# Performance work log

Measured on AMD Instinct MI355X. Metric: run time of the kernel, lower is better.

The kernel has to match this reference:

```python
import jax, jax.numpy as jnp
import numpy as np

NUM_EMBED = 1024
EMBED_DIM = 256
DECAY = 0.99
EPS = 1e-05
COMMIT = 0.25


def setup_inputs() -> dict:
    key = jax.random.key(0)
    k1, k2, k3 = jax.random.split(key, 3)
    z = jax.random.normal(k1, (64, 32, 32, EMBED_DIM), dtype=jnp.float32)
    lim = 1.0 / NUM_EMBED
    embeddings = jax.random.uniform(k2, (NUM_EMBED, EMBED_DIM), minval=-lim, maxval=lim, dtype=jnp.float32)
    ema_embed = jax.random.uniform(k3, (NUM_EMBED, EMBED_DIM), minval=-lim, maxval=lim, dtype=jnp.float32)
    cluster_size = jnp.zeros((NUM_EMBED,), dtype=jnp.float32)
    return {"z": z, "embeddings": embeddings, "ema_embed": ema_embed, "cluster_size": cluster_size}


def reference(z, embeddings, ema_embed, cluster_size):
    B, H, W, D = z.shape
    zf = z.reshape(-1, D)  # [N, D]
    # squared euclidean distances to codebook: [N, K]
    distances = (zf ** 2).sum(-1, keepdims=True) + (embeddings ** 2).sum(-1) - 2.0 * (zf @ embeddings.T)
    closest = jnp.argmin(distances, axis=-1)  # [N] int
    quantized_indices = closest.reshape(B, H, W)[:, None]  # [B,1,H,W]
    quantized = embeddings[closest].reshape(z.shape)  # gather instead of one-hot GEMM

    # --- training-mode EMA codebook update (buffer math, no grads) ---
    n_i = jnp.zeros((NUM_EMBED,), dtype=zf.dtype).at[closest].add(1.0)  # per-code counts
    new_cluster = cluster_size * DECAY + n_i * (1.0 - DECAY)
    dw = jnp.zeros_like(embeddings).at[closest].add(zf)  # scatter-add of assigned vectors
    new_ema = ema_embed * DECAY + dw * (1.0 - DECAY)
    n = new_cluster.sum()
    new_cluster = (new_cluster + EPS) / (n + NUM_EMBED * EPS) * n
    new_embeddings = new_ema / new_cluster[:, None]

    commitment_loss = jnp.mean((quantized - z) ** 2)
    st_quantized = z + jax.lax.stop_gradient(quantized - z)  # straight-through
    loss = commitment_loss * COMMIT
    return loss, st_quantized, quantized_indices, new_embeddings, new_cluster, new_ema
```

## Files before the change

kernel.cpp:

```cpp
#include <hip/hip_runtime.h>
#include <float.h>
#include <stdint.h>

#define K_EMB 1024
#define D_EMB 256

typedef _Float16 half8 __attribute__((ext_vector_type(8)));
typedef float f32x4_t __attribute__((ext_vector_type(4)));


__global__ void convert_e_kernel(const float* __restrict__ e, _Float16* __restrict__ ehp,
                                 float* __restrict__ t2, unsigned int* __restrict__ flag_cnt) {
  if (blockIdx.x == 0 && threadIdx.x == 0) { flag_cnt[0] = 0; flag_cnt[1] = 0; }
  int row = blockIdx.x * 4 + (threadIdx.x >> 6);
  int lane = threadIdx.x & 63;
  float4 v = ((const float4*)(e + (size_t)row * D_EMB))[lane];
  float s = v.x * v.x + v.y * v.y + v.z * v.z + v.w * v.w;
#pragma unroll
  for (int off = 32; off > 0; off >>= 1) s += __shfl_down(s, off, 64);
  if (lane == 0) t2[row] = s;
  _Float16* dst = ehp + (size_t)row * D_EMB + lane * 4;
  dst[0] = (_Float16)v.x; dst[1] = (_Float16)v.y;
  dst[2] = (_Float16)v.z; dst[3] = (_Float16)v.w;
}


#define BM 256
#define CCH 64
#define NCH (K_EMB / CCH)
#define DELTA 1.5e-4f

__launch_bounds__(512, 2)
__global__ void argmin_mfma_kernel(const float* __restrict__ z,
                                   const _Float16* __restrict__ eh,
                                   const float* __restrict__ t2,
                                   int* __restrict__ closest,
                                   float* __restrict__ idx_out,
                                   unsigned int* __restrict__ flag_cnt,
                                   unsigned int* __restrict__ flag_row,
                                   unsigned int* __restrict__ flag_cand) {
  __shared__ _Float16 ebuf[2 * CCH * D_EMB];
  const int tid = threadIdx.x;
  const int wid = tid >> 6;
  const int lane = tid & 63;
  const int c = lane & 15, g = lane >> 4;
  const int row0 = blockIdx.x * BM + wid * 32;

  half8 A[2][8];
#pragma unroll
  for (int fr = 0; fr < 2; ++fr)
#pragma unroll
    for (int df = 0; df < 8; ++df) {
      const float* zp = z + (size_t)(row0 + fr * 16 + c) * D_EMB + df * 32 + g * 8;
      const float4 v0 = *(const float4*)zp;
      const float4 v1 = *(const float4*)(zp + 4);
      half8 h;
      h[0] = (_Float16)v0.x; h[1] = (_Float16)v0.y; h[2] = (_Float16)v0.z; h[3] = (_Float16)v0.w;
      h[4] = (_Float16)v1.x; h[5] = (_Float16)v1.y; h[6] = (_Float16)v1.z; h[7] = (_Float16)v1.w;
      A[fr][df] = h;
    }

  float m1[8], m2[8], m3[8];
  int k1[8], k2[8];
#pragma unroll
  for (int s = 0; s < 8; ++s) { m1[s] = FLT_MAX; m2[s] = FLT_MAX; m3[s] = FLT_MAX; k1[s] = 0; k2[s] = 0; }

#define INS(s, dvv, kkv)                                        \
  {                                                             \
    const float dv_ = (dvv); const int kk_ = (kkv);             \
    const bool lt1 = dv_ < m1[s];                               \
    const bool lt2 = dv_ < m2[s];                               \
    m3[s] = __builtin_amdgcn_fmed3f(m2[s], m3[s], dv_);         \
    const float nm2 = __builtin_amdgcn_fmed3f(m1[s], m2[s], dv_); \
    k2[s] = lt1 ? k1[s] : (lt2 ? kk_ : k2[s]);                  \
    m2[s] = nm2;                                                \
    m1[s] = fminf(m1[s], dv_);                                  \
    k1[s] = lt1 ? kk_ : k1[s];                                  \
  }

  const int scode = tid >> 3;
  const int s8 = tid & 7;
  const int swz_w = (scode & 7) << 3;
  const int rswz = (c & 7) << 3;

  half8 st[4];
  {
    const _Float16* src = eh + (size_t)scode * D_EMB + s8 * 8;
#pragma unroll
    for (int u = 0; u < 4; ++u) st[u] = *(const half8*)(src + u * 64);
    _Float16* dst = ebuf + scode * D_EMB;
#pragma unroll
    for (int u = 0; u < 4; ++u) {
      const int elem = (s8 * 8 + u * 64) ^ swz_w;
      *(half8*)(dst + elem) = st[u];
    }
  }

  int cur = 0;
  for (int cb = 0; cb < NCH; ++cb) {
    __syncthreads();

    if (cb + 1 < NCH) {
      const _Float16* src = eh + (size_t)((cb + 1) * CCH + scode) * D_EMB + s8 * 8;
#pragma unroll
      for (int u = 0; u < 4; ++u) st[u] = *(const half8*)(src + u * 64);
    }

    const _Float16* rb = ebuf + cur * (CCH * D_EMB);
    f32x4_t acc[2][4];
#pragma unroll
    for (int fr = 0; fr < 2; ++fr)
#pragma unroll
      for (int fc = 0; fc < 4; ++fc) acc[fr][fc] = (f32x4_t){0.f, 0.f, 0.f, 0.f};

#pragma unroll
    for (int d = 0; d < 8; ++d) {
      half8 Bh[4];
#pragma unroll
      for (int fc = 0; fc < 4; ++fc) {
        const int elem = (d * 32 + g * 8) ^ rswz;
        Bh[fc] = *(const half8*)(rb + (fc * 16 + c) * D_EMB + elem);
      }
#pragma unroll
      for (int fr = 0; fr < 2; ++fr)
#pragma unroll
        for (int fc = 0; fc < 4; ++fc)
          acc[fr][fc] = __builtin_amdgcn_mfma_f32_16x16x32_f16(A[fr][d], Bh[fc], acc[fr][fc], 0, 0, 0);
    }

    if (cb + 1 < NCH) {
      _Float16* dst = ebuf + (cur ^ 1) * (CCH * D_EMB) + scode * D_EMB;
#pragma unroll
      for (int u = 0; u < 4; ++u) {
        const int elem = (s8 * 8 + u * 64) ^ swz_w;
        *(half8*)(dst + elem) = st[u];
      }
    }

#pragma unroll
    for (int fc = 0; fc < 4; ++fc) {
      const int kk = cb * CCH + fc * 16 + c;
      const float t2c = t2[kk];
#pragma unroll
      for (int fr = 0; fr < 2; ++fr)
#pragma unroll
        for (int r = 0; r < 4; ++r) {
          const float dv = fmaf(-2.f, acc[fr][fc][r], t2c);
          const int s = fr * 4 + r;
          INS(s, dv, kk)
        }
    }
    cur ^= 1;
  }

#pragma unroll
  for (int m = 1; m <= 8; m <<= 1) {
#pragma unroll
    for (int s = 0; s < 8; ++s) {
      const float om1 = __shfl_xor(m1[s], m, 64);
      const int ok1 = __shfl_xor(k1[s], m, 64);
      const float om2 = __shfl_xor(m2[s], m, 64);
      const int ok2 = __shfl_xor(k2[s], m, 64);
      const float om3 = __shfl_xor(m3[s], m, 64);
      INS(s, om1, ok1)
      INS(s, om2, ok2)
      m3[s] = fminf(m3[s], om3);
    }
  }
#undef INS

  if (c == 0) {
#pragma unroll
    for (int s = 0; s < 8; ++s) {
      const int fr = s >> 2, r = s & 3;
      const int row = row0 + fr * 16 + g * 4 + r;
      closest[row] = k1[s];
      idx_out[row] = (float)k1[s];
      if (m2[s] - m1[s] < DELTA) {
        const unsigned int p = atomicAdd(flag_cnt, 1u);
        flag_row[p] = (unsigned int)row;
        flag_cand[p] = (unsigned int)k1[s] | ((unsigned int)k2[s] << 10) |
                       ((m3[s] - m1[s] < DELTA) ? (1u << 20) : 0u);
      }
    }
  }
}


__launch_bounds__(256, 4)
__global__ void fixup_pair_kernel(const float* __restrict__ z, const float* __restrict__ emb,
                                  const float* __restrict__ t2,
                                  const unsigned int* __restrict__ flag_cnt,
                                  const unsigned int* __restrict__ flag_row,
                                  const unsigned int* __restrict__ flag_cand,
                                  int* __restrict__ closest, float* __restrict__ idx_out,
                                  unsigned int* __restrict__ flag2_cnt,
                                  unsigned int* __restrict__ flag2) {
  const int tid = threadIdx.x;
  const int q = tid & 3;
  const unsigned int cnt = *flag_cnt;
  const unsigned int nquads = (gridDim.x * 256) >> 2;
  for (unsigned int i = (blockIdx.x * 256 + tid) >> 2; i < cnt; i += nquads) {
    const int row = (int)flag_row[i];
    const unsigned int cand = flag_cand[i];
    if ((cand >> 20) & 1u) {
      if (q == 0) {
        const unsigned int p = atomicAdd(flag2_cnt, 1u);
        flag2[p] = (unsigned int)row;
      }
      continue;
    }
    const int ka = (int)(cand & 1023u), kb = (int)((cand >> 10) & 1023u);
    const float4* zp = (const float4*)(z + (size_t)row * D_EMB) + q * 16;
    const float4* ap = (const float4*)(emb + (size_t)ka * D_EMB) + q * 16;
    const float4* bp = (const float4*)(emb + (size_t)kb * D_EMB) + q * 16;
    float s0 = 0.f, sa = 0.f, sb = 0.f;
#pragma unroll 8
    for (int u = 0; u < 16; ++u) {
      const float4 zv = zp[u], av = ap[u], bv = bp[u];
      s0 = fmaf(zv.x, zv.x, s0); s0 = fmaf(zv.y, zv.y, s0);
      s0 = fmaf(zv.z, zv.z, s0); s0 = fmaf(zv.w, zv.w, s0);
      sa = fmaf(zv.x, av.x, sa); sa = fmaf(zv.y, av.y, sa);
      sa = fmaf(zv.z, av.z, sa); sa = fmaf(zv.w, av.w, sa);
      sb = fmaf(zv.x, bv.x, sb); sb = fmaf(zv.y, bv.y, sb);
      sb = fmaf(zv.z, bv.z, sb); sb = fmaf(zv.w, bv.w, sb);
    }
#pragma unroll
    for (int m = 1; m <= 2; m <<= 1) {
      s0 += __shfl_xor(s0, m, 64);
      sa += __shfl_xor(sa, m, 64);
      sb += __shfl_xor(sb, m, 64);
    }
    if (q == 0) {
      const float da = (s0 + t2[ka]) - 2.f * sa;
      const float db = (s0 + t2[kb]) - 2.f * sb;
      int kbest = ka;
      if (db < da || (db == da && kb < ka)) kbest = kb;
      closest[row] = kbest;
      idx_out[row] = (float)kbest;
    }
  }
}


__launch_bounds__(256, 4)
__global__ void fixup_full_kernel(const float* __restrict__ z, const float* __restrict__ emb,
                                  const float* __restrict__ t2,
                                  const unsigned int* __restrict__ flag2_cnt,
                                  const unsigned int* __restrict__ flag2,
                                  int* __restrict__ closest, float* __restrict__ idx_out) {
  __shared__ float zs[D_EMB];
  __shared__ float t1s;
  __shared__ float redm[4];
  __shared__ int redk[4];
  const int tid = threadIdx.x;
  const int lane = tid & 63, wv = tid >> 6;
  const unsigned int cnt = *flag2_cnt;
  for (unsigned int j = blockIdx.x; j < cnt; j += gridDim.x) {
    __syncthreads();
    const int row = (int)flag2[j];
    if (wv == 0) {
      const float4 v = ((const float4*)(z + (size_t)row * D_EMB))[lane];
      ((float4*)zs)[lane] = v;
      float s = v.x * v.x + v.y * v.y + v.z * v.z + v.w * v.w;
#pragma unroll
      for (int off = 32; off > 0; off >>= 1) s += __shfl_down(s, off, 64);
      if (lane == 0) t1s = s;
    }
    __syncthreads();
    const float4* e0 = (const float4*)(emb + (size_t)(4 * tid + 0) * D_EMB);
    const float4* e1 = (const float4*)(emb + (size_t)(4 * tid + 1) * D_EMB);
    const float4* e2 = (const float4*)(emb + (size_t)(4 * tid + 2) * D_EMB);
    const float4* e3 = (const float4*)(emb + (size_t)(4 * tid + 3) * D_EMB);
    const float4* zp4 = (const float4*)zs;
    float a0 = 0.f, a1 = 0.f, a2 = 0.f, a3 = 0.f;
    for (int i = 0; i < 64; ++i) {
      const float4 z4 = zp4[i];
      const float4 v0 = e0[i], v1 = e1[i], v2 = e2[i], v3 = e3[i];
      a0 = fmaf(z4.x, v0.x, a0); a0 = fmaf(z4.y, v0.y, a0);
      a0 = fmaf(z4.z, v0.z, a0); a0 = fmaf(z4.w, v0.w, a0);
      a1 = fmaf(z4.x, v1.x, a1); a1 = fmaf(z4.y, v1.y, a1);
      a1 = fmaf(z4.z, v1.z, a1); a1 = fmaf(z4.w, v1.w, a1);
      a2 = fmaf(z4.x, v2.x, a2); a2 = fmaf(z4.y, v2.y, a2);
      a2 = fmaf(z4.z, v2.z, a2); a2 = fmaf(z4.w, v2.w, a2);
      a3 = fmaf(z4.x, v3.x, a3); a3 = fmaf(z4.y, v3.y, a3);
      a3 = fmaf(z4.z, v3.z, a3); a3 = fmaf(z4.w, v3.w, a3);
    }
    const float t1v = t1s;
    float best = FLT_MAX;
    int bk = 0x7fffffff;
    const float dvs[4] = {(t1v + t2[4 * tid + 0]) - 2.f * a0,
                          (t1v + t2[4 * tid + 1]) - 2.f * a1,
                          (t1v + t2[4 * tid + 2]) - 2.f * a2,
                          (t1v + t2[4 * tid + 3]) - 2.f * a3};
#pragma unroll
    for (int cc = 0; cc < 4; ++cc) {
      const int k = 4 * tid + cc;
      if (dvs[cc] < best) { best = dvs[cc]; bk = k; }
    }
#pragma unroll
    for (int m = 1; m <= 32; m <<= 1) {
      const float ob = __shfl_xor(best, m, 64);
      const int ok = __shfl_xor(bk, m, 64);
      if (ob < best || (ob == best && ok < bk)) { best = ob; bk = ok; }
    }
    if (lane == 0) { redm[wv] = best; redk[wv] = bk; }
    __syncthreads();
    if (tid == 0) {
      float b = redm[0];
      int k = redk[0];
#pragma unroll
      for (int w = 1; w < 4; ++w)
        if (redm[w] < b || (redm[w] == b && redk[w] < k)) { b = redm[w]; k = redk[w]; }
      closest[row] = k;
      idx_out[row] = (float)k;
    }
  }
}


__global__ void hist1_kernel(const int* __restrict__ closest, unsigned int* __restrict__ rank,
                             unsigned int* __restrict__ blockhist) {
  __shared__ unsigned int lh[K_EMB];
  const int t = threadIdx.x;
  lh[t] = 0;
  __syncthreads();
  const int row = blockIdx.x * 1024 + t;
  rank[row] = atomicAdd(&lh[closest[row]], 1u);
  __syncthreads();
  blockhist[blockIdx.x * K_EMB + t] = lh[t];
}

__global__ void hist2_kernel(unsigned int* __restrict__ blockhist, const float* __restrict__ cs,
                             unsigned int* __restrict__ base, float* __restrict__ newc,
                             float* __restrict__ o_ncl, int nblocks) {
  __shared__ unsigned int sc[K_EMB];
  __shared__ float fr[K_EMB];
  const int bin = threadIdx.x;
  unsigned int s = 0;
  for (int b = 0; b < nblocks; ++b) {
    const unsigned int v = blockhist[b * K_EMB + bin];
    blockhist[b * K_EMB + bin] = s;
    s += v;
  }
  sc[bin] = s;
  __syncthreads();
  for (int off = 1; off < K_EMB; off <<= 1) {
    const unsigned int t = (bin >= off) ? sc[bin - off] : 0u;
    __syncthreads();
    sc[bin] += t;
    __syncthreads();
  }
  base[bin] = sc[bin] - s;
  const float pre = cs[bin] * 0.99f + (float)s * (float)(1.0 - 0.99);
  fr[bin] = pre;
  __syncthreads();
  for (int st = 512; st > 0; st >>= 1) {
    if (bin < st) fr[bin] += fr[bin + st];
    __syncthreads();
  }
  const float n = fr[0];
  const float ncl = (pre + 1e-5f) / (n + (float)(K_EMB * 1e-5)) * n;
  newc[bin] = ncl;
  o_ncl[bin] = ncl;
}

__global__ void hist3_kernel(const int* __restrict__ closest, const unsigned int* __restrict__ rank,
                             const unsigned int* __restrict__ blockhist,
                             const unsigned int* __restrict__ base,
                             unsigned int* __restrict__ sorted) {
  const int t = threadIdx.x;
  const int row = blockIdx.x * 1024 + t;
  const int k = closest[row];
  sorted[base[k] + blockhist[blockIdx.x * K_EMB + k] + rank[row]] = (unsigned int)row;
}


__global__ void dwsum_kernel(const float* __restrict__ z, const unsigned int* __restrict__ sorted,
                             const unsigned int* __restrict__ base, const float* __restrict__ ema,
                             const float* __restrict__ newc, const float* __restrict__ emb,
                             float* __restrict__ o_st, float* __restrict__ o_nema,
                             float* __restrict__ o_nemb, float* __restrict__ loss_part, int N) {
  const int k = blockIdx.x;
  const int lane = threadIdx.x & 63, wv = threadIdx.x >> 6;
  const unsigned int b0 = base[k];
  const unsigned int b1 = (k == K_EMB - 1) ? (unsigned int)N : base[k + 1];
  const float4 ev = ((const float4*)(emb + (size_t)k * D_EMB))[lane];
  float4 acc = {0.f, 0.f, 0.f, 0.f};
  float ls = 0.f;
  for (unsigned int j = b0 + wv; j < b1; j += 4) {
    const unsigned int row = sorted[j];
    const float4 zv = ((const float4*)(z + (size_t)row * D_EMB))[lane];
    const float dx = ev.x - zv.x, dy = ev.y - zv.y, dz = ev.z - zv.z, dww = ev.w - zv.w;
    float* sp = o_st + (size_t)row * D_EMB + lane * 4;
    sp[0] = zv.x + dx; sp[1] = zv.y + dy; sp[2] = zv.z + dz; sp[3] = zv.w + dww;
    ls = fmaf(dx, dx, ls); ls = fmaf(dy, dy, ls);
    ls = fmaf(dz, dz, ls); ls = fmaf(dww, dww, ls);
    acc.x += zv.x; acc.y += zv.y; acc.z += zv.z; acc.w += zv.w;
  }
  __shared__ float4 red[256];
  __shared__ float lred[256];
  red[threadIdx.x] = acc;
  lred[threadIdx.x] = ls;
  __syncthreads();
  for (int s = 128; s > 0; s >>= 1) {
    if (threadIdx.x < s) lred[threadIdx.x] += lred[threadIdx.x + s];
    __syncthreads();
  }
  if (threadIdx.x == 0) loss_part[k] = lred[0];
  if (wv == 0) {
    const float4 a1 = red[64 + lane], a2 = red[128 + lane], a3 = red[192 + lane];
    acc = red[lane];
    acc.x += a1.x + a2.x + a3.x;
    acc.y += a1.y + a2.y + a3.y;
    acc.z += a1.z + a2.z + a3.z;
    acc.w += a1.w + a2.w + a3.w;
    const float4 emv = ((const float4*)ema)[k * 64 + lane];
    const float nc = newc[k];
    const int off = k * D_EMB + lane * 4;
    float ne;
    ne = emv.x * 0.99f + acc.x * (float)(1.0 - 0.99); o_nema[off + 0] = ne; o_nemb[off + 0] = ne / nc;
    ne = emv.y * 0.99f + acc.y * (float)(1.0 - 0.99); o_nema[off + 1] = ne; o_nemb[off + 1] = ne / nc;
    ne = emv.z * 0.99f + acc.z * (float)(1.0 - 0.99); o_nema[off + 2] = ne; o_nemb[off + 2] = ne / nc;
    ne = emv.w * 0.99f + acc.w * (float)(1.0 - 0.99); o_nema[off + 3] = ne; o_nemb[off + 3] = ne / nc;
  }
}

__global__ void loss_final_kernel(const float* __restrict__ loss_part,
                                  float* __restrict__ o_loss, int nrows) {
  const int i = threadIdx.x;
  __shared__ double dred[1024];
  dred[i] = (double)loss_part[i];
  __syncthreads();
  for (int s = 512; s > 0; s >>= 1) {
    if (i < s) dred[i] += dred[i + s];
    __syncthreads();
  }
  if (i == 0) o_loss[0] = (float)(0.25 * (dred[0] / ((double)nrows * (double)D_EMB)));
}


extern "C" void kernel_launch(void* const* d_in, const int* in_sizes, int n_in,
                              void* d_out, int out_size, void* d_ws, size_t ws_size,
                              hipStream_t stream) {
  const float* z = (const float*)d_in[0];
  const float* emb = (const float*)d_in[1];
  const float* ema = (const float*)d_in[2];
  const float* cs = (const float*)d_in[3];
  const int N = in_sizes[0] / D_EMB;
  const int NB = N / 1024;

  float* out = (float*)d_out;
  float* o_loss = out;
  float* o_st = out + 1;
  float* o_idx = o_st + (size_t)N * D_EMB;
  float* o_nemb = o_idx + N;
  float* o_ncl = o_nemb + (size_t)K_EMB * D_EMB;
  float* o_nema = o_ncl + K_EMB;

  float* ws = (float*)d_ws;
  float* t2 = ws;
  float* newc = t2 + K_EMB;
  float* loss_part = newc + K_EMB;
  unsigned int* flag_cnt = (unsigned int*)(loss_part + K_EMB);
  unsigned int* basep = flag_cnt + 4;
  _Float16* ehp = (_Float16*)(basep + K_EMB);
  int* closest = (int*)(ehp + (size_t)K_EMB * D_EMB);
  unsigned int* flag_row = (unsigned int*)(closest + N);
  unsigned int* flag_cand = flag_row + N;
  unsigned int* sorted = flag_cand + N;
  unsigned int* flag2 = sorted + N;

  unsigned int* rank = flag_row;
  unsigned int* blockhist = flag_cand;
  unsigned int* flag2_cnt = flag_cnt + 1;

  convert_e_kernel<<<K_EMB / 4, 256, 0, stream>>>(emb, ehp, t2, flag_cnt);
  argmin_mfma_kernel<<<N / BM, 512, 0, stream>>>(z, ehp, t2, closest, o_idx,
                                                 flag_cnt, flag_row, flag_cand);
  fixup_pair_kernel<<<128, 256, 0, stream>>>(z, emb, t2, flag_cnt, flag_row, flag_cand,
                                             closest, o_idx, flag2_cnt, flag2);
  fixup_full_kernel<<<128, 256, 0, stream>>>(z, emb, t2, flag2_cnt, flag2, closest, o_idx);
  hist1_kernel<<<NB, 1024, 0, stream>>>(closest, rank, blockhist);
  hist2_kernel<<<1, 1024, 0, stream>>>(blockhist, cs, basep, newc, o_ncl, NB);
  hist3_kernel<<<NB, 1024, 0, stream>>>(closest, rank, blockhist, basep, sorted);
  dwsum_kernel<<<K_EMB, 256, 0, stream>>>(z, sorted, basep, ema, newc, emb,
                                          o_st, o_nema, o_nemb, loss_part, N);
  loss_final_kernel<<<1, 1024, 0, stream>>>(loss_part, o_loss, N);
}
```

Before: 199.3 us.

## Stream codebook chunks via global_load_lds with smaller tiles in argmin kernel

```diff
diff --git a/kernel.cpp b/kernel.cpp
--- a/kernel.cpp
+++ b/kernel.cpp
@@ -7,6 +7,9 @@
 
 typedef _Float16 half8 __attribute__((ext_vector_type(8)));
 typedef float f32x4_t __attribute__((ext_vector_type(4)));
+
+typedef const __attribute__((address_space(1))) void* as1cv;
+typedef __attribute__((address_space(3))) void* as3v;
 
 
 __global__ void convert_e_kernel(const float* __restrict__ e, _Float16* __restrict__ ehp,
@@ -25,12 +28,12 @@
 }
 
 
-#define BM 256
-#define CCH 64
+#define BM 128
+#define CCH 32
 #define NCH (K_EMB / CCH)
 #define DELTA 1.5e-4f
 
-__launch_bounds__(512, 2)
+__launch_bounds__(256, 3)
 __global__ void argmin_mfma_kernel(const float* __restrict__ z,
                                    const _Float16* __restrict__ eh,
                                    const float* __restrict__ t2,
@@ -39,7 +42,7 @@
                                    unsigned int* __restrict__ flag_cnt,
                                    unsigned int* __restrict__ flag_row,
                                    unsigned int* __restrict__ flag_cand) {
-  __shared__ _Float16 ebuf[2 * CCH * D_EMB];
+  __shared__ _Float16 ebuf[2][CCH * D_EMB];
   const int tid = threadIdx.x;
   const int wid = tid >> 6;
   const int lane = tid & 63;
@@ -78,67 +81,55 @@
     k1[s] = lt1 ? kk_ : k1[s];                                  \
   }
 
-  const int scode = tid >> 3;
-  const int s8 = tid & 7;
-  const int swz_w = (scode & 7) << 3;
   const int rswz = (c & 7) << 3;
 
-  half8 st[4];
-  {
-    const _Float16* src = eh + (size_t)scode * D_EMB + s8 * 8;
-#pragma unroll
-    for (int u = 0; u < 4; ++u) st[u] = *(const half8*)(src + u * 64);
-    _Float16* dst = ebuf + scode * D_EMB;
-#pragma unroll
-    for (int u = 0; u < 4; ++u) {
-      const int elem = (s8 * 8 + u * 64) ^ swz_w;
-      *(half8*)(dst + elem) = st[u];
-    }
-  }
+  int sgs[4];
+#pragma unroll
+  for (int u = 0; u < 4; ++u) {
+    const int gidx = (wid * 4 + u) * 64 + lane;
+    sgs[u] = (gidx & ~7) | ((gidx & 7) ^ ((gidx >> 5) & 7));
+  }
+
+#pragma unroll
+  for (int u = 0; u < 4; ++u)
+    __builtin_amdgcn_global_load_lds((as1cv)(eh + (size_t)sgs[u] * 8),
+                                     (as3v)(&ebuf[0][(wid * 4 + u) * 512]), 16, 0, 0);
 
   int cur = 0;
   for (int cb = 0; cb < NCH; ++cb) {
     __syncthreads();
 
     if (cb + 1 < NCH) {
-      const _Float16* src = eh + (size_t)((cb + 1) * CCH + scode) * D_EMB + s8 * 8;
-#pragma unroll
-      for (int u = 0; u < 4; ++u) st[u] = *(const half8*)(src + u * 64);
-    }
-
-    const _Float16* rb = ebuf + cur * (CCH * D_EMB);
-    f32x4_t acc[2][4];
+      const _Float16* src0 = eh + (size_t)(cb + 1) * (CCH * D_EMB);
+#pragma unroll
+      for (int u = 0; u < 4; ++u)
+        __builtin_amdgcn_global_load_lds((as1cv)(src0 + (size_t)sgs[u] * 8),
+                                         (as3v)(&ebuf[cur ^ 1][(wid * 4 + u) * 512]), 16, 0, 0);
+    }
+
+    f32x4_t acc[2][2];
 #pragma unroll
     for (int fr = 0; fr < 2; ++fr)
 #pragma unroll
-      for (int fc = 0; fc < 4; ++fc) acc[fr][fc] = (f32x4_t){0.f, 0.f, 0.f, 0.f};
+      for (int fc = 0; fc < 2; ++fc) acc[fr][fc] = (f32x4_t){0.f, 0.f, 0.f, 0.f};
 
 #pragma unroll
     for (int d = 0; d < 8; ++d) {
-      half8 Bh[4];
-#pragma unroll
-      for (int fc = 0; fc < 4; ++fc) {
+      half8 Bh[2];
+#pragma unroll
+      for (int fc = 0; fc < 2; ++fc) {
         const int elem = (d * 32 + g * 8) ^ rswz;
-        Bh[fc] = *(const half8*)(rb + (fc * 16 + c) * D_EMB + elem);
+        Bh[fc] = *(const half8*)(&ebuf[cur][(fc * 16 + c) * D_EMB + elem]);
       }
 #pragma unroll
       for (int fr = 0; fr < 2; ++fr)
 #pragma unroll
-        for (int fc = 0; fc < 4; ++fc)
+        for (int fc = 0; fc < 2; ++fc)
           acc[fr][fc] = __builtin_amdgcn_mfma_f32_16x16x32_f16(A[fr][d], Bh[fc], acc[fr][fc], 0, 0, 0);
     }
 
-    if (cb + 1 < NCH) {
-      _Float16* dst = ebuf + (cur ^ 1) * (CCH * D_EMB) + scode * D_EMB;
-#pragma unroll
-      for (int u = 0; u < 4; ++u) {
-        const int elem = (s8 * 8 + u * 64) ^ swz_w;
-        *(half8*)(dst + elem) = st[u];
-      }
-    }
-
-#pragma unroll
-    for (int fc = 0; fc < 4; ++fc) {
+#pragma unroll
+    for (int fc = 0; fc < 2; ++fc) {
       const int kk = cb * CCH + fc * 16 + c;
       const float t2c = t2[kk];
 #pragma unroll
@@ -476,7 +467,7 @@
   unsigned int* flag2_cnt = flag_cnt + 1;
 
   convert_e_kernel<<<K_EMB / 4, 256, 0, stream>>>(emb, ehp, t2, flag_cnt);
-  argmin_mfma_kernel<<<N / BM, 512, 0, stream>>>(z, ehp, t2, closest, o_idx,
+  argmin_mfma_kernel<<<N / BM, 256, 0, stream>>>(z, ehp, t2, closest, o_idx,
                                                  flag_cnt, flag_row, flag_cand);
   fixup_pair_kernel<<<128, 256, 0, stream>>>(z, emb, t2, flag_cnt, flag_row, flag_cand,
                                              closest, o_idx, flag2_cnt, flag2);
```

After: 194.1 us. 1.03x faster.
